# Kernel tuning notes

Hardware: AMD Instinct MI355X
Metric: run time of the kernel (lower is better)

Reference implementation:

```python
import jax, jax.numpy as jnp
import numpy as np

LAYER_VEC = [2000, 200, 100, 10]
EN_DIMS = [(2000, 200), (200, 100), (100, 10)]      # (num_in, num_out) per encoder FC_layer
DE_DIMS = [(10, 100), (100, 200), (200, 2000)]      # decoder is reversed
EN_SIZES = [ni * no + no for ni, no in EN_DIMS]     # [400200, 20100, 1010] -> 421310
DE_SIZES = [ni * no + no for ni, no in DE_DIMS]     # [1100, 20200, 402000] -> 423300
ACT_VEC = ['linear', 'tanh', 'linear']              # ['linear'] + (len-3)*[activation] + ['linear']


def _hyper(mu, W0, b0, W1, b1, W2, b2):
    # nn.Sequential: Linear -> tanh -> Linear -> tanh -> Linear (depth_hyper=2)
    h = jnp.tanh(mu @ W0.T + b0)
    h = jnp.tanh(h @ W1.T + b1)
    return h @ W2.T + b2  # [B, param_size]


def _fc_layer(x, p, num_in, num_out):
    # FC_layer.forward: per-sample weight matvec + bias
    B = x.shape[0]
    w = p[:, :num_out * num_in].reshape(B, num_out, num_in)
    b = p[:, num_out * num_in:]
    return jnp.einsum('ab,acb->ac', x, w) + b


def _act(x, name):
    return jnp.tanh(x) if name == 'tanh' else x


def _run_stack(data, params, dims, sizes):
    cut = 0
    for (ni, no), sz, a in zip(dims, sizes, ACT_VEC):
        data = _act(_fc_layer(data, params[:, cut:cut + sz], ni, no), a)
        cut += sz
    return data


def setup_inputs() -> dict:
    key = jax.random.key(0)
    ks = jax.random.split(key, 16)
    B, NS, W = 64, 4, 64
    EN_P, DE_P = sum(EN_SIZES), sum(DE_SIZES)
    f32 = jnp.float32
    inp = {
        'z':  jax.random.normal(ks[0], (B, LAYER_VEC[0]), f32),
        'mu': jax.random.normal(ks[1], (B, NS), f32),
        'en_W0': jax.random.normal(ks[2], (W, NS), f32) / np.sqrt(NS),
        'en_b0': jnp.zeros((W,), f32),
        'en_W1': jax.random.normal(ks[3], (W, W), f32) / np.sqrt(W),
        'en_b1': jnp.zeros((W,), f32),
        'en_W2': jax.random.normal(ks[4], (EN_P, W), f32) * 0.01,
        'en_b2': jnp.zeros((EN_P,), f32),
        'de_W0': jax.random.normal(ks[5], (W, NS), f32) / np.sqrt(NS),
        'de_b0': jnp.zeros((W,), f32),
        'de_W1': jax.random.normal(ks[6], (W, W), f32) / np.sqrt(W),
        'de_b1': jnp.zeros((W,), f32),
        'de_W2': jax.random.normal(ks[7], (DE_P, W), f32) * 0.01,
        'de_b2': jnp.zeros((DE_P,), f32),
    }
    return inp


def reference(z, mu, en_W0, en_b0, en_W1, en_b1, en_W2, en_b2,
              de_W0, de_b0, de_W1, de_b1, de_W2, de_b2):
    # encode
    p_en = _hyper(mu, en_W0, en_b0, en_W1, en_b1, en_W2, en_b2)
    x = _run_stack(z, p_en, EN_DIMS, EN_SIZES)
    # decode
    p_de = _hyper(mu, de_W0, de_b0, de_W1, de_b1, de_W2, de_b2)
    z_reconst = _run_stack(x, p_de, DE_DIMS, DE_SIZES)
    return (z_reconst, x)
```

## Files before the change

### kernel.cpp

```cpp
#include <hip/hip_runtime.h>
#include <stdint.h>


__global__ __launch_bounds__(256) void prep_kernel(
    const float* __restrict__ z, const float* __restrict__ mu,
    const float* __restrict__ enW0, const float* __restrict__ enb0,
    const float* __restrict__ enW1, const float* __restrict__ enb1,
    const float* __restrict__ deW0, const float* __restrict__ deb0,
    const float* __restrict__ deW1, const float* __restrict__ deb1,
    float* __restrict__ zT, float* __restrict__ hen, float* __restrict__ hde)
{
    __shared__ float tile[64 * 65];
    __shared__ float h0s[4][64];
    const int bid  = blockIdx.x;
    const int lane = threadIdx.x & 63;
    const int g    = threadIdx.x >> 6;

    if (bid < 32) {
        const int t0 = bid * 64;
        for (int bb = g; bb < 64; bb += 4) {
            int i = t0 + lane;
            tile[bb * 65 + lane] = (i < 2000) ? z[bb * 2000 + i] : 0.f;
        }
        __syncthreads();
        for (int ii = g; ii < 64; ii += 4) {
            int i = t0 + ii;
            if (i < 2000) zT[i * 64 + lane] = tile[lane * 65 + ii];
        }
    } else {
        const int task  = (bid - 32) * 4 + g;
        const int which = task >> 6;
        const int b     = task & 63;
        const float* W0 = which ? deW0 : enW0;
        const float* b0 = which ? deb0 : enb0;
        const float* W1 = which ? deW1 : enW1;
        const float* b1 = which ? deb1 : enb1;
        float* hout     = which ? hde : hen;
        const int j = lane;
        float m0 = mu[b * 4 + 0], m1 = mu[b * 4 + 1], m2 = mu[b * 4 + 2], m3 = mu[b * 4 + 3];
        float v = tanhf(m0 * W0[j * 4 + 0] + m1 * W0[j * 4 + 1] +
                        m2 * W0[j * 4 + 2] + m3 * W0[j * 4 + 3] + b0[j]);
        h0s[g][j] = v;
        __syncthreads();
        float a = b1[j];
        const float* W1r = W1 + j * 64;
        #pragma unroll 8
        for (int k = 0; k < 64; ++k) a = fmaf(h0s[g][k], W1r[k], a);
        hout[b * 64 + j] = tanhf(a);
    }
}

__device__ __forceinline__ void gload16(const float* g, float* l)
{
    __builtin_amdgcn_global_load_lds(
        (const __attribute__((address_space(1))) void*)g,
        (__attribute__((address_space(3))) void*)l,
        16, 0, 0);
}

template <int NI, int NO, int NSPLIT, bool TANH, bool ATOMIC>
__global__ __launch_bounds__(256, 8) void fc_kernel(
    const float* __restrict__ xT,
    const float* __restrict__ h,
    const float* __restrict__ W2,
    const float* __restrict__ b2,
    float* __restrict__ yT)
{
    const int lane = threadIdx.x & 63;
    const int wave = threadIdx.x >> 6;
    const int kg   = lane & 15;
    const int bgl  = lane >> 4;
    const int b0   = wave * 16 + bgl * 4;

    const int o = blockIdx.x % NO;
    const int s = blockIdx.x / NO;
    constexpr int CH = NI / NSPLIT;
    const int i0   = s * CH;
    const int iend = i0 + CH;

    constexpr int  TR     = 20;
    constexpr bool STAGED = (CH >= TR) && (CH % TR == 0);
    constexpr int  NT     = STAGED ? (CH / TR) : 1;
    constexpr int  CHUNKS = TR / 4;

    __shared__ float Wl[STAGED ? 2 * TR * 64 : 4];
    __shared__ float Xl[STAGED ? 2 * TR * 64 : 4];

    float acc[4][4];
    #pragma unroll
    for (int a = 0; a < 4; ++a)
        #pragma unroll
        for (int c = 0; c < 4; ++c) acc[a][c] = 0.f;

    auto fma16 = [&](const float4& w, const float4& x) {
        acc[0][0] = fmaf(x.x, w.x, acc[0][0]);
        acc[0][1] = fmaf(x.x, w.y, acc[0][1]);
        acc[0][2] = fmaf(x.x, w.z, acc[0][2]);
        acc[0][3] = fmaf(x.x, w.w, acc[0][3]);
        acc[1][0] = fmaf(x.y, w.x, acc[1][0]);
        acc[1][1] = fmaf(x.y, w.y, acc[1][1]);
        acc[1][2] = fmaf(x.y, w.z, acc[1][2]);
        acc[1][3] = fmaf(x.y, w.w, acc[1][3]);
        acc[2][0] = fmaf(x.z, w.x, acc[2][0]);
        acc[2][1] = fmaf(x.z, w.y, acc[2][1]);
        acc[2][2] = fmaf(x.z, w.z, acc[2][2]);
        acc[2][3] = fmaf(x.z, w.w, acc[2][3]);
        acc[3][0] = fmaf(x.w, w.x, acc[3][0]);
        acc[3][1] = fmaf(x.w, w.y, acc[3][1]);
        acc[3][2] = fmaf(x.w, w.z, acc[3][2]);
        acc[3][3] = fmaf(x.w, w.w, acc[3][3]);
    };

    if constexpr (STAGED) {
        const float* __restrict__ Wg = W2 + ((size_t)o * NI + i0) * 64;
        const float* __restrict__ xg = xT + (size_t)i0 * 64;

        auto STAGE = [&](int bufn, int tt) {
            const float* ws = Wg + (size_t)tt * TR * 64;
            const float* xs = xg + (size_t)tt * TR * 64;
            float* wl = &Wl[bufn * (TR * 64)];
            float* xl = &Xl[bufn * (TR * 64)];
            for (int c = wave; c < CHUNKS; c += 4) {
                gload16(ws + c * 256 + lane * 4, wl + c * 256);
                gload16(xs + c * 256 + lane * 4, xl + c * 256);
            }
        };

        STAGE(0, 0);
        __syncthreads();

        int buf = 0;
        for (int t = 0; t < NT; ++t) {
            if (t + 1 < NT) STAGE(buf ^ 1, t + 1);
            const float* wl = &Wl[buf * (TR * 64)];
            const float* xl = &Xl[buf * (TR * 64)];
            #pragma unroll
            for (int r = 0; r < TR; ++r) {
                const float4 w = *(const float4*)(wl + r * 64 + 4 * kg);
                const float4 x = *(const float4*)(xl + r * 64 + b0);
                fma16(w, x);
            }
            __syncthreads();
            buf ^= 1;
        }
    } else {
        const float4* __restrict__ wq = (const float4*)(W2 + ((size_t)o * NI + i0) * 64) + kg;
        const float4* __restrict__ xq = (const float4*)(xT + (size_t)i0 * 64) + (wave * 4 + bgl);
        #pragma unroll
        for (int i = 0; i < CH; ++i) fma16(wq[i * 16], xq[i * 16]);
    }

    const float* __restrict__ b2w = b2 + (size_t)o * NI;
    float xb[4] = {0.f, 0.f, 0.f, 0.f};
    constexpr int T16 = (CH + 15) / 16;
    #pragma unroll 4
    for (int t = 0; t < T16; ++t) {
        const int ib = i0 + t * 16 + kg;
        if (ib < iend) {
            const float  bv = b2w[ib];
            const float4 xv = *(const float4*)(xT + (size_t)ib * 64 + b0);
            xb[0] = fmaf(xv.x, bv, xb[0]);
            xb[1] = fmaf(xv.y, bv, xb[1]);
            xb[2] = fmaf(xv.z, bv, xb[2]);
            xb[3] = fmaf(xv.w, bv, xb[3]);
        }
    }

    float4 wb = make_float4(0.f, 0.f, 0.f, 0.f);
    if (!ATOMIC || s == 0)
        wb = *(const float4*)(W2 + ((size_t)NO * NI + o) * 64 + 4 * kg);

    float out0, out1, out2, out3;
    #pragma unroll
    for (int a = 0; a < 4; ++a) {
        const float4 hv = *(const float4*)(h + (size_t)(b0 + a) * 64 + 4 * kg);
        float v = xb[a];
        v = fmaf(hv.x, acc[a][0] + wb.x, v);
        v = fmaf(hv.y, acc[a][1] + wb.y, v);
        v = fmaf(hv.z, acc[a][2] + wb.z, v);
        v = fmaf(hv.w, acc[a][3] + wb.w, v);
        v += __shfl_xor(v, 1, 64);
        v += __shfl_xor(v, 2, 64);
        v += __shfl_xor(v, 4, 64);
        v += __shfl_xor(v, 8, 64);
        if (a == 0) out0 = v;
        else if (a == 1) out1 = v;
        else if (a == 2) out2 = v;
        else out3 = v;
    }

    if (kg < 4) {
        float v = out0;
        v = (kg == 1) ? out1 : v;
        v = (kg == 2) ? out2 : v;
        v = (kg == 3) ? out3 : v;
        const int b = b0 + kg;
        if (!ATOMIC || s == 0) v += b2[(size_t)NO * NI + o];
        if (TANH) v = tanhf(v);
        if (ATOMIC) atomicAdd(&yT[o * 64 + b], v);
        else        yT[o * 64 + b] = v;
    }
}

__global__ __launch_bounds__(256) void final_kernel(
    const float* __restrict__ d3,
    const float* __restrict__ y3,
    float* __restrict__ out)
{
    int t = blockIdx.x * 256 + threadIdx.x;
    if (t < 128000) {
        int b = t / 2000, oo = t - b * 2000;
        out[t] = d3[oo * 64 + b];
    } else if (t < 128640) {
        int u = t - 128000;
        int b = u / 10, oo = u - b * 10;
        out[t] = y3[oo * 64 + b];
    }
}

extern "C" void kernel_launch(void* const* d_in, const int* in_sizes, int n_in,
                              void* d_out, int out_size, void* d_ws, size_t ws_size,
                              hipStream_t stream)
{
    const float* z    = (const float*)d_in[0];
    const float* mu   = (const float*)d_in[1];
    const float* enW0 = (const float*)d_in[2];
    const float* enb0 = (const float*)d_in[3];
    const float* enW1 = (const float*)d_in[4];
    const float* enb1 = (const float*)d_in[5];
    const float* enW2 = (const float*)d_in[6];
    const float* enb2 = (const float*)d_in[7];
    const float* deW0 = (const float*)d_in[8];
    const float* deb0 = (const float*)d_in[9];
    const float* deW1 = (const float*)d_in[10];
    const float* deb1 = (const float*)d_in[11];
    const float* deW2 = (const float*)d_in[12];
    const float* deb2 = (const float*)d_in[13];

    float* ws  = (float*)d_ws;
    float* zT  = ws;
    float* hen = zT + 128000;
    float* hde = hen + 4096;
    float* y1  = hde + 4096;
    float* y2  = y1 + 200 * 64;
    float* y3  = y2 + 100 * 64;
    float* d1  = y3 + 10 * 64;
    float* d2  = d1 + 100 * 64;
    float* d3  = d2 + 200 * 64;
    float* out = (float*)d_out;

    hipMemsetAsync(y1, 0, 200 * 64 * sizeof(float), stream);
    hipMemsetAsync(y3, 0, 10 * 64 * sizeof(float), stream);
    prep_kernel<<<64, 256, 0, stream>>>(z, mu, enW0, enb0, enW1, enb1,
                                        deW0, deb0, deW1, deb1, zT, hen, hde);
    fc_kernel<2000, 200, 10, false, true ><<<2000, 256, 0, stream>>>(zT, hen, enW2, enb2, y1);
    fc_kernel< 200, 100,  1, true,  false><<< 100, 256, 0, stream>>>(y1, hen, enW2 + (size_t)400200 * 64, enb2 + 400200, y2);
    fc_kernel< 100,  10, 10, false, true ><<< 100, 256, 0, stream>>>(y2, hen, enW2 + (size_t)420300 * 64, enb2 + 420300, y3);
    fc_kernel<  10, 100,  1, false, false><<< 100, 256, 0, stream>>>(y3, hde, deW2, deb2, d1);
    fc_kernel< 100, 200,  1, true,  false><<< 200, 256, 0, stream>>>(d1, hde, deW2 + (size_t)1100 * 64, deb2 + 1100, d2);
    fc_kernel< 200, 2000, 1, false, false><<<2000, 256, 0, stream>>>(d2, hde, deW2 + (size_t)21300 * 64, deb2 + 21300, d3);

    final_kernel<<<(128640 + 255) / 256, 256, 0, stream>>>(d3, y3, out);
}
```

Baseline: 357.4 us.

## Triple-buffer FC staging with two loads in flight and explicit vmcnt waits

Replaces the double-buffered LDS staging in the per-sample FC kernel with a three-buffer ring that keeps two tiles in flight. Each iteration waits with an explicit s_waitcnt vmcnt(10) plus a raw s_barrier, where the old code used a full __syncthreads, so more global latency can overlap compute. The direct-to-LDS loads change from 16-byte to 4-byte transfers, giving four times as many load instructions. Staging now applies only when a chunk holds at least two tiles. The extra buffer raises LDS use per block, which may cut occupancy.

```diff
diff --git a/kernel.cpp b/kernel.cpp
--- a/kernel.cpp
+++ b/kernel.cpp
@@ -50,12 +50,12 @@
     }
 }
 
-__device__ __forceinline__ void gload16(const float* g, float* l)
+__device__ __forceinline__ void gload4(const float* g, float* l)
 {
     __builtin_amdgcn_global_load_lds(
         (const __attribute__((address_space(1))) void*)g,
         (__attribute__((address_space(3))) void*)l,
-        16, 0, 0);
+        4, 0, 0);
 }
 
 template <int NI, int NO, int NSPLIT, bool TANH, bool ATOMIC>
@@ -79,12 +79,11 @@
     const int iend = i0 + CH;
 
     constexpr int  TR     = 20;
-    constexpr bool STAGED = (CH >= TR) && (CH % TR == 0);
+    constexpr bool STAGED = (CH >= 2 * TR) && (CH % TR == 0);
     constexpr int  NT     = STAGED ? (CH / TR) : 1;
-    constexpr int  CHUNKS = TR / 4;
-
-    __shared__ float Wl[STAGED ? 2 * TR * 64 : 4];
-    __shared__ float Xl[STAGED ? 2 * TR * 64 : 4];
+
+    __shared__ float Wl[STAGED ? 3 * TR * 64 : 4];
+    __shared__ float Xl[STAGED ? 3 * TR * 64 : 4];
 
     float acc[4][4];
     #pragma unroll
@@ -120,29 +119,41 @@
             const float* xs = xg + (size_t)tt * TR * 64;
             float* wl = &Wl[bufn * (TR * 64)];
             float* xl = &Xl[bufn * (TR * 64)];
-            for (int c = wave; c < CHUNKS; c += 4) {
-                gload16(ws + c * 256 + lane * 4, wl + c * 256);
-                gload16(xs + c * 256 + lane * 4, xl + c * 256);
+            #pragma unroll
+            for (int c = 0; c < 5; ++c) {
+                const int cc = c * 4 + wave;
+                gload4(ws + cc * 64 + lane, wl + cc * 64);
+                gload4(xs + cc * 64 + lane, xl + cc * 64);
             }
         };
 
-        STAGE(0, 0);
-        __syncthreads();
-
-        int buf = 0;
-        for (int t = 0; t < NT; ++t) {
-            if (t + 1 < NT) STAGE(buf ^ 1, t + 1);
-            const float* wl = &Wl[buf * (TR * 64)];
-            const float* xl = &Xl[buf * (TR * 64)];
+        auto COMPUTE = [&](int bufn) {
+            const float* wl = &Wl[bufn * (TR * 64)];
+            const float* xl = &Xl[bufn * (TR * 64)];
             #pragma unroll
             for (int r = 0; r < TR; ++r) {
                 const float4 w = *(const float4*)(wl + r * 64 + 4 * kg);
                 const float4 x = *(const float4*)(xl + r * 64 + b0);
                 fma16(w, x);
             }
-            __syncthreads();
-            buf ^= 1;
-        }
+        };
+
+        STAGE(0, 0);
+        STAGE(1, 1);
+        int buf = 0;
+        for (int t = 0; t < NT - 1; ++t) {
+            asm volatile("s_waitcnt vmcnt(10)" ::: "memory");
+            __builtin_amdgcn_s_barrier();
+            if (t + 2 < NT) {
+                int nb = buf + 2; if (nb >= 3) nb -= 3;
+                STAGE(nb, t + 2);
+            }
+            COMPUTE(buf);
+            buf = (buf == 2) ? 0 : buf + 1;
+        }
+        asm volatile("s_waitcnt vmcnt(0)" ::: "memory");
+        __builtin_amdgcn_s_barrier();
+        COMPUTE(buf);
     } else {
         const float4* __restrict__ wq = (const float4*)(W2 + ((size_t)o * NI + i0) * 64) + kg;
         const float4* __restrict__ xq = (const float4*)(xT + (size_t)i0 * 64) + (wave * 4 + bgl);
```

After: 558.7 us. 56.3% more time.

## Add register-tiled fc8 kernel with double-buffered LDS staging for large layers

Applied to the files above, without the earlier changes.

Adds a new kernel for the two large FC layers (2000->200 and 200->2000). Each wave computes one output neuron, and each lane accumulates an 8x8 register tile over hidden units and batch rows. Weight and input tiles are staged into double-buffered shared memory with async 16-byte loads. Blocks now cover four outputs each, so each weight tile is loaded once and reused across the whole batch, which should cut memory traffic and raise arithmetic intensity. The cost is heavy register pressure, 64 accumulators plus launch_bounds(256,3), and fewer blocks in the grid.

```diff
diff --git a/kernel.cpp b/kernel.cpp
--- a/kernel.cpp
+++ b/kernel.cpp
@@ -202,6 +202,136 @@
     }
 }
 
+template <int NI, int NO, int NSPLIT, bool TANH, bool ATOMIC>
+__global__ __launch_bounds__(256, 3) void fc8_kernel(
+    const float* __restrict__ xT,
+    const float* __restrict__ h,
+    const float* __restrict__ W2,
+    const float* __restrict__ b2,
+    float* __restrict__ yT)
+{
+    const int lane = threadIdx.x & 63;
+    const int wave = threadIdx.x >> 6;
+    const int kg   = lane & 7;
+    const int bgl  = lane >> 3;
+
+    constexpr int OQ = NO / 4;
+    const int oq = blockIdx.x % OQ;
+    const int s  = blockIdx.x / OQ;
+    const int o  = oq * 4 + wave;
+    constexpr int CH = NI / NSPLIT;
+    const int i0 = s * CH;
+
+    constexpr int TR = 20;
+    constexpr int NT = CH / TR;
+
+    __shared__ float Wl[2][4][TR * 64];
+    __shared__ float Xl[2][TR * 64];
+
+    float acc[8][8];
+    #pragma unroll
+    for (int kk = 0; kk < 8; ++kk)
+        #pragma unroll
+        for (int bb = 0; bb < 8; ++bb) acc[kk][bb] = 0.f;
+
+    auto STAGE = [&](int bf, int tt) {
+        const int bi = i0 + tt * TR;
+        #pragma unroll
+        for (int c = 0; c < 5; ++c) {
+            const int cc = c * 4 + wave;
+            const int ol = cc / 5, rb = cc % 5;
+            gload16(W2 + ((size_t)(oq * 4 + ol) * NI + bi + rb * 4) * 64 + lane * 4,
+                    &Wl[bf][ol][rb * 256]);
+        }
+        for (int c2 = wave; c2 < 5; c2 += 4)
+            gload16(xT + (size_t)(bi + c2 * 4) * 64 + lane * 4, &Xl[bf][c2 * 256]);
+    };
+
+    auto COMPUTE = [&](int bf) {
+        const float* __restrict__ wl = &Wl[bf][wave][0];
+        const float* __restrict__ xl = &Xl[bf][0];
+        #pragma unroll
+        for (int r = 0; r < TR; ++r) {
+            const float4 wA = *(const float4*)(wl + r * 64 + kg * 8);
+            const float4 wB = *(const float4*)(wl + r * 64 + kg * 8 + 4);
+            const float4 xA = *(const float4*)(xl + r * 64 + bgl * 8);
+            const float4 xB = *(const float4*)(xl + r * 64 + bgl * 8 + 4);
+            const float wv[8] = {wA.x, wA.y, wA.z, wA.w, wB.x, wB.y, wB.z, wB.w};
+            const float xv[8] = {xA.x, xA.y, xA.z, xA.w, xB.x, xB.y, xB.z, xB.w};
+            #pragma unroll
+            for (int kk = 0; kk < 8; ++kk)
+                #pragma unroll
+                for (int bb = 0; bb < 8; ++bb)
+                    acc[kk][bb] = fmaf(xv[bb], wv[kk], acc[kk][bb]);
+        }
+    };
+
+    STAGE(0, 0);
+    __syncthreads();
+    int buf = 0;
+    for (int t = 0; t < NT; ++t) {
+        if (t + 1 < NT) STAGE(buf ^ 1, t + 1);
+        COMPUTE(buf);
+        __syncthreads();
+        buf ^= 1;
+    }
+
+    const float* __restrict__ b2w = b2 + (size_t)o * NI;
+    float xb[8];
+    #pragma unroll
+    for (int bb = 0; bb < 8; ++bb) xb[bb] = 0.f;
+    constexpr int T8 = (CH + 7) / 8;
+    #pragma unroll 4
+    for (int t = 0; t < T8; ++t) {
+        const int ib = i0 + t * 8 + kg;
+        if (ib < i0 + CH) {
+            const float  bv = b2w[ib];
+            const float4 xA = *(const float4*)(xT + (size_t)ib * 64 + bgl * 8);
+            const float4 xB = *(const float4*)(xT + (size_t)ib * 64 + bgl * 8 + 4);
+            xb[0] = fmaf(xA.x, bv, xb[0]);
+            xb[1] = fmaf(xA.y, bv, xb[1]);
+            xb[2] = fmaf(xA.z, bv, xb[2]);
+            xb[3] = fmaf(xA.w, bv, xb[3]);
+            xb[4] = fmaf(xB.x, bv, xb[4]);
+            xb[5] = fmaf(xB.y, bv, xb[5]);
+            xb[6] = fmaf(xB.z, bv, xb[6]);
+            xb[7] = fmaf(xB.w, bv, xb[7]);
+        }
+    }
+
+    float wbv[8] = {0.f, 0.f, 0.f, 0.f, 0.f, 0.f, 0.f, 0.f};
+    if (!ATOMIC || s == 0) {
+        const float4 wbA = *(const float4*)(W2 + ((size_t)NO * NI + o) * 64 + kg * 8);
+        const float4 wbB = *(const float4*)(W2 + ((size_t)NO * NI + o) * 64 + kg * 8 + 4);
+        wbv[0] = wbA.x; wbv[1] = wbA.y; wbv[2] = wbA.z; wbv[3] = wbA.w;
+        wbv[4] = wbB.x; wbv[5] = wbB.y; wbv[6] = wbB.z; wbv[7] = wbB.w;
+    }
+
+    float myv = 0.f;
+    #pragma unroll
+    for (int bb = 0; bb < 8; ++bb) {
+        const int b = bgl * 8 + bb;
+        const float4 hA = *(const float4*)(h + (size_t)b * 64 + kg * 8);
+        const float4 hB = *(const float4*)(h + (size_t)b * 64 + kg * 8 + 4);
+        const float hv[8] = {hA.x, hA.y, hA.z, hA.w, hB.x, hB.y, hB.z, hB.w};
+        float v = xb[bb];
+        #pragma unroll
+        for (int kk = 0; kk < 8; ++kk)
+            v = fmaf(hv[kk], acc[kk][bb] + wbv[kk], v);
+        v += __shfl_xor(v, 1, 64);
+        v += __shfl_xor(v, 2, 64);
+        v += __shfl_xor(v, 4, 64);
+        if (kg == bb) myv = v;
+    }
+
+    const int b = bgl * 8 + kg;
+    float outv = myv;
+    if (!ATOMIC || s == 0) outv += b2[(size_t)NO * NI + o];
+    if (TANH) outv = tanhf(outv);
+    if (ATOMIC) atomicAdd(&yT[o * 64 + b], outv);
+    else        yT[o * 64 + b] = outv;
+}
+
 __global__ __launch_bounds__(256) void final_kernel(
     const float* __restrict__ d3,
     const float* __restrict__ y3,
@@ -253,12 +383,12 @@
     hipMemsetAsync(y3, 0, 10 * 64 * sizeof(float), stream);
     prep_kernel<<<64, 256, 0, stream>>>(z, mu, enW0, enb0, enW1, enb1,
                                         deW0, deb0, deW1, deb1, zT, hen, hde);
-    fc_kernel<2000, 200, 10, false, true ><<<2000, 256, 0, stream>>>(zT, hen, enW2, enb2, y1);
-    fc_kernel< 200, 100,  1, true,  false><<< 100, 256, 0, stream>>>(y1, hen, enW2 + (size_t)400200 * 64, enb2 + 400200, y2);
-    fc_kernel< 100,  10, 10, false, true ><<< 100, 256, 0, stream>>>(y2, hen, enW2 + (size_t)420300 * 64, enb2 + 420300, y3);
-    fc_kernel<  10, 100,  1, false, false><<< 100, 256, 0, stream>>>(y3, hde, deW2, deb2, d1);
-    fc_kernel< 100, 200,  1, true,  false><<< 200, 256, 0, stream>>>(d1, hde, deW2 + (size_t)1100 * 64, deb2 + 1100, d2);
-    fc_kernel< 200, 2000, 1, false, false><<<2000, 256, 0, stream>>>(d2, hde, deW2 + (size_t)21300 * 64, deb2 + 21300, d3);
+    fc8_kernel<2000, 200, 10, false, true ><<<(200/4) * 10, 256, 0, stream>>>(zT, hen, enW2, enb2, y1);
+    fc_kernel < 200, 100,  1, true,  false><<< 100, 256, 0, stream>>>(y1, hen, enW2 + (size_t)400200 * 64, enb2 + 400200, y2);
+    fc_kernel < 100,  10, 10, false, true ><<< 100, 256, 0, stream>>>(y2, hen, enW2 + (size_t)420300 * 64, enb2 + 420300, y3);
+    fc_kernel <  10, 100,  1, false, false><<< 100, 256, 0, stream>>>(y3, hde, deW2, deb2, d1);
+    fc_kernel < 100, 200,  1, true,  false><<< 200, 256, 0, stream>>>(d1, hde, deW2 + (size_t)1100 * 64, deb2 + 1100, d2);
+    fc8_kernel< 200, 2000, 1, false, false><<<2000/4, 256, 0, stream>>>(d2, hde, deW2 + (size_t)21300 * 64, deb2 + 21300, d3);
 
     final_kernel<<<(128640 + 255) / 256, 256, 0, stream>>>(d3, y3, out);
 }
```

Result: slower. 537.8 us (+50.5%).
